# Kernel tuning notes

Measured on AMD Instinct MI355X. Metric: run time of the kernel, lower is better.

The kernel has to match this reference:

```python
import jax, jax.numpy as jnp
import numpy as np
from jax import lax

B, C_IN, H, W = 32, 96, 48, 48
D = C_IN          # d_inner = expand(1) * in_features
K, N, DT_RANK = 2, 16, 6   # k_group, d_state, ceil(D/16)


def setup_inputs() -> dict:
    key = jax.random.key(0)
    ks = jax.random.split(key, 10)
    s = 0.02
    return {
        "x": jax.random.normal(ks[0], (B, C_IN, H, W), jnp.float32),
        "in_proj_w": jax.random.normal(ks[1], (D, C_IN)) * s,
        "in_proj_b": jnp.zeros((D,)),
        "skip_w": jax.random.normal(ks[2], (1, 1, 5)) * s,
        "skip_b": jnp.zeros((1,)),
        "conv2d_w": jax.random.normal(ks[3], (D, 1, 3, 3)) * s,
        "conv2d_b": jnp.zeros((D,)),
        "local_w": jax.random.normal(ks[4], (D, 1, 3, 3)) * s,
        "local_b": jnp.zeros((D,)),
        "bn_gamma": jnp.ones((D,)),
        "bn_beta": jnp.zeros((D,)),
        "x_proj_w": jax.random.normal(ks[5], (K, DT_RANK + 2 * N, D)) * s,
        "dt_projs_w": jax.random.normal(ks[6], (K, D, DT_RANK)) * s,
        "dt_projs_b": jax.random.normal(ks[7], (K, D)) * s,
        "A_logs": jnp.tile(jnp.log(jnp.arange(1, N + 1, dtype=jnp.float32))[None], (K * D, 1)),
        "Ds": jnp.ones((K * D,)),
        "norm_gamma": jnp.ones((D,)),
        "norm_beta": jnp.zeros((D,)),
        "out_proj_w": jax.random.normal(ks[8], (C_IN, D)) * s,
        "out_proj_b": jnp.zeros((C_IN,)),
    }


def _dwconv2d(x, w, bias):
    # depthwise 3x3, NCHW
    y = lax.conv_general_dilated(x, w, (1, 1), "SAME", feature_group_count=x.shape[1],
                                 dimension_numbers=("NCHW", "OIHW", "NCHW"))
    return y + bias[None, :, None, None]


def _forward(x, in_proj_w, in_proj_b, skip_w, skip_b, conv2d_w, conv2d_b,
             local_w, local_b, bn_gamma, bn_beta, x_proj_w, dt_projs_w,
             dt_projs_b, A_logs, Ds, norm_gamma, norm_beta, out_proj_w, out_proj_b):
    b, c, h, w = x.shape
    L = h * w
    x_in = jnp.transpose(x, (0, 2, 3, 1))                       # [B,H,W,C]
    # skip gate: Conv1d(1,1,k=5) over channel axis of the spatial mean
    zm = jnp.mean(x_in, axis=(1, 2))[:, None, :]                # [B,1,C]
    z = lax.conv_general_dilated(zm, skip_w, (1,), "SAME",
                                 dimension_numbers=("NCH", "OIH", "NCH")) + skip_b[None, :, None]
    z = z[:, None]                                              # [B,1,1,C]
    x_feat = jnp.transpose(x_in @ in_proj_w.T + in_proj_b, (0, 3, 1, 2))  # [B,D,H,W]
    x_conv = jax.nn.silu(_dwconv2d(x_feat, conv2d_w, conv2d_b))
    # ---- dynamic center-similarity ordering (computed under no_grad) ----
    xc = lax.stop_gradient(x_conv)
    xf = xc.reshape(b, D, L)
    xn = xf / jnp.maximum(jnp.linalg.norm(xf, axis=1, keepdims=True), 1e-12)
    cf = xc[:, :, h // 2, w // 2]                               # [B,D]
    cn = cf / jnp.maximum(jnp.linalg.norm(cf, axis=1, keepdims=True), 1e-12)
    sim = jnp.einsum("bdl,bd->bl", xn, cn)
    sort_idx = jnp.argsort(-sim, axis=1)                        # descending similarity
    inv_idx = jnp.argsort(sort_idx, axis=1)
    # ---- DynamicCenterScan: sorted sequence and its reverse (k_group=2) ----
    xseq = jnp.take_along_axis(x_conv.reshape(b, D, L), sort_idx[:, None, :], axis=2)
    xs = jnp.stack([xseq, jnp.flip(xseq, -1)], axis=1)          # [B,K,D,L]
    # ---- SS2D selective-scan core ----
    x_dbl = jnp.einsum("bkdl,kcd->bkcl", xs, x_proj_w)
    dts, Bs, Cs = jnp.split(x_dbl, [DT_RANK, DT_RANK + N], axis=2)
    dts = jnp.einsum("bkrl,kdr->bkdl", dts, dt_projs_w)
    dts = jax.nn.softplus(dts + dt_projs_b[None, :, :, None])   # [B,K,D,L]
    A = -jnp.exp(A_logs.reshape(K, D, N))                       # [K,D,N]

    def step(hst, t):
        dt_l, B_l, C_l, x_l = t                                 # [B,K,D],[B,K,N],[B,K,N],[B,K,D]
        dA = jnp.exp(dt_l[..., None] * A)                       # [B,K,D,N]
        hst = dA * hst + (dt_l * x_l)[..., None] * B_l[:, :, None, :]
        y = jnp.einsum("bkdn,bkn->bkd", hst, C_l)
        return hst, y

    tmove = lambda a: jnp.moveaxis(a, -1, 0)
    h0 = jnp.zeros((b, K, D, N), x.dtype)
    _, ys_t = lax.scan(step, h0, (tmove(dts), tmove(Bs), tmove(Cs), tmove(xs)))
    ys = jnp.moveaxis(ys_t, 0, -1) + Ds.reshape(K, D)[None, :, :, None] * xs  # [B,K,D,L]
    # ---- DynamicCenterMerge: un-flip, sum directions, inverse permutation ----
    y = ys[:, 0] + jnp.flip(ys[:, 1], -1)
    y = jnp.take_along_axis(y, inv_idx[:, None, :], axis=2).reshape(b, D, h, w)
    # out_norm: LayerNorm over channels
    yl = jnp.transpose(y, (0, 2, 3, 1))
    mu = jnp.mean(yl, -1, keepdims=True)
    var = jnp.var(yl, -1, keepdims=True)
    yl = (yl - mu) / jnp.sqrt(var + 1e-5) * norm_gamma + norm_beta
    out_mamba = jnp.transpose(yl, (0, 3, 1, 2))
    # local path: depthwise conv + BatchNorm (batch stats, train mode) + SiLU
    lc = _dwconv2d(x_conv, local_w, local_b)
    bm = jnp.mean(lc, (0, 2, 3))
    bv = jnp.var(lc, (0, 2, 3))
    lc = (lc - bm[None, :, None, None]) * (bn_gamma / jnp.sqrt(bv + 1e-5))[None, :, None, None] + bn_beta[None, :, None, None]
    lc = jax.nn.silu(lc)
    out = out_mamba + lc
    # softmax over dim=1 of z (singleton) == all-ones gate; kept for faithfulness
    out = jnp.transpose(out, (0, 2, 3, 1)) * jax.nn.softmax(z, axis=1)
    out = out @ out_proj_w.T + out_proj_b
    return jnp.transpose(out, (0, 3, 1, 2))


def reference(x, in_proj_w, in_proj_b, skip_w, skip_b, conv2d_w, conv2d_b,
              local_w, local_b, bn_gamma, bn_beta, x_proj_w, dt_projs_w,
              dt_projs_b, A_logs, Ds, norm_gamma, norm_beta, out_proj_w, out_proj_b):
    return _forward(x, in_proj_w, in_proj_b, skip_w, skip_b, conv2d_w, conv2d_b,
                    local_w, local_b, bn_gamma, bn_beta, x_proj_w, dt_projs_w,
                    dt_projs_b, A_logs, Ds, norm_gamma, norm_beta, out_proj_w, out_proj_b)
```

## Files before the change

kernel.cpp:

```cpp
#include <hip/hip_runtime.h>
#include <hip/hip_bf16.h>


typedef __hip_bfloat16 bf16;
typedef float v2f __attribute__((ext_vector_type(2)));
typedef float v4f __attribute__((ext_vector_type(4)));
#define SH2(V, a, b) __builtin_shufflevector(V, V, a, b)

__device__ __forceinline__ float b2f(bf16 v) { return __bfloat162float(v); }
__device__ __forceinline__ float ldu(const void* p, int i, bool f32) {
  if (f32) return ((const float*)p)[i];
  return b2f(((const bf16*)p)[i]);
}
__device__ __forceinline__ float rcp_f(float x) { return __builtin_amdgcn_rcpf(x); }

#define LL 2304
#define NSEG 72

#define W_INT  0
#define B_IN   9216
#define W_C2D  9312
#define B_C2D  10176
#define W_LOC  10272
#define B_LOC  11136
#define BN_G   11232
#define BN_B   11328
#define W_XPT  11424
#define W_DT   19104
#define B_DT   20256
#define A2OF   20448
#define DSOF   23520
#define LN_G   23712
#define LN_B   23808
#define W_OUTT 23904
#define B_OUT  33120
#define WBUF_N 33280ul

#define O_WBUF  0ul
#define O_XFEAT 33280ul
#define O_XCONV 7111168ul
#define O_SIM   14189056ul
#define O_SIDX  14262784ul
#define O_XST   14336512ul
#define O_XSTD  21414400ul
#define O_RBUF  28492288ul
#define O_BC    29671936ul
#define O_DSUM  34390528ul
#define O_YMLM  34832896ul
#define O_STATS 41910784ul
#define O_AFLG  41910976ul
#define O_SCSH  41911040ul
#define O_FLAG  41911232ul
#define O_END   41911296ul

__global__ void k_detect(const void* x, float* flag) {
  int i = threadIdx.x;
  bool bad = false;
  const bf16* xb = (const bf16*)x;
#pragma unroll
  for (int r = 0; r < 4; ++r) {
    float v = b2f(xb[r * 64 + i]);
    if (!(fabsf(v) <= 1e4f)) bad = true;
  }
  bool any = __any(bad);
  if (i == 0) flag[0] = any ? 1.f : 0.f;
}

__global__ void k_prep(const void* ipw, const void* ipb, const void* c2w, const void* c2b,
                       const void* lw, const void* lb, const void* bng, const void* bnb,
                       const void* xpw, const void* dtw, const void* dtb, const void* alog,
                       const void* dss, const void* ng, const void* nb, const void* opw,
                       const void* opb, float* wb, const float* flag, float* aflag) {
  bool f = flag[0] > 0.5f;
  int i = blockIdx.x * 256 + threadIdx.x;
  if (i < 9216) {
    int r = i / 96, c = i % 96;
    wb[W_INT + c * 96 + r] = ldu(ipw, i, f);
    wb[W_OUTT + c * 96 + r] = ldu(opw, i, f);
  }
  if (i < 96) {
    wb[B_IN + i] = ldu(ipb, i, f); wb[B_C2D + i] = ldu(c2b, i, f); wb[B_LOC + i] = ldu(lb, i, f);
    wb[BN_G + i] = ldu(bng, i, f); wb[BN_B + i] = ldu(bnb, i, f); wb[LN_G + i] = ldu(ng, i, f);
    wb[LN_B + i] = ldu(nb, i, f); wb[B_OUT + i] = ldu(opb, i, f);
  }
  if (i < 864) { wb[W_C2D + i] = ldu(c2w, i, f); wb[W_LOC + i] = ldu(lw, i, f); }
  if (i < 7296) {
    int k = i / 3648, c = (i / 96) % 38, d = i % 96;
    wb[W_XPT + d * 80 + k * 38 + c] = ldu(xpw, i, f);
  }
  if (i < 1152) wb[W_DT + i] = ldu(dtw, i, f);
  if (i < 192) { wb[B_DT + i] = ldu(dtb, i, f); wb[DSOF + i] = ldu(dss, i, f); }
  if (i < 3072) {
    float av = expf(ldu(alog, i, f));
    wb[A2OF + i] = -av * 1.4426950408889634f;
    int n = i % 16;
    if (fabsf(av - (float)(n + 1)) > 1e-3f * (n + 1)) atomicAdd(aflag, 1.f);
  }
}

__global__ __launch_bounds__(128, 4)
void k_inproj(const void* __restrict__ x, const float* __restrict__ wb,
              float* __restrict__ xfeat, const float* __restrict__ flag) {
  int b = blockIdx.x / 72;
  int rest = blockIdx.x % 72;
  int q = rest / 18;
  int l = (rest % 18) * 128 + threadIdx.x;
  float acc[24];
#pragma unroll
  for (int j = 0; j < 24; ++j) acc[j] = wb[B_IN + q * 24 + j];
  bool f = flag[0] > 0.5f;
  if (f) {
    const float* xf = (const float*)x;
#pragma unroll 2
    for (int c = 0; c < 96; ++c) {
      float xc = xf[(b * 96 + c) * LL + l];
      const float* wr = wb + W_INT + c * 96 + q * 24;
#pragma unroll
      for (int j = 0; j < 24; ++j) acc[j] += xc * wr[j];
    }
  } else {
    const bf16* xb = (const bf16*)x;
#pragma unroll 2
    for (int c = 0; c < 96; ++c) {
      float xc = b2f(xb[(b * 96 + c) * LL + l]);
      const float* wr = wb + W_INT + c * 96 + q * 24;
#pragma unroll
      for (int j = 0; j < 24; ++j) acc[j] += xc * wr[j];
    }
  }
#pragma unroll
  for (int j = 0; j < 24; ++j) xfeat[(b * 96 + q * 24 + j) * LL + l] = acc[j];
}

__global__ __launch_bounds__(256, 8)
void k_conv_silu(const float* __restrict__ xfeat, const float* __restrict__ wb,
                 float* __restrict__ xconv) {
  int t = blockIdx.x * 256 + threadIdx.x;
  int l = t % LL; int d = (t / LL) % 96; int b = t / (LL * 96);
  int h = l / 48, w = l % 48;
  const float* wr = wb + W_C2D + d * 9;
  const float* src = xfeat + (b * 96 + d) * LL;
  float acc = wb[B_C2D + d];
#pragma unroll
  for (int ki = 0; ki < 3; ++ki) {
    int hh = h + ki - 1; if (hh < 0 || hh >= 48) continue;
#pragma unroll
    for (int kj = 0; kj < 3; ++kj) {
      int ww = w + kj - 1; if (ww < 0 || ww >= 48) continue;
      acc += src[hh * 48 + ww] * wr[ki * 3 + kj];
    }
  }
  xconv[t] = acc / (1.f + expf(-acc));
}

__global__ __launch_bounds__(256, 8)
void k_sim(const float* __restrict__ xconv, float* __restrict__ sim) {
  int b = blockIdx.x / 9;
  int l = (blockIdx.x % 9) * 256 + threadIdx.x;
  const float* base = xconv + (size_t)b * 96 * LL;
  float dot = 0, nrm = 0, cn = 0;
  for (int d = 0; d < 96; ++d) {
    float v = base[d * LL + l];
    float c = base[d * LL + 1176];
    dot += v * c; nrm += v * v; cn += c * c;
  }
  float den = fmaxf(sqrtf(nrm), 1e-12f) * fmaxf(sqrtf(cn), 1e-12f);
  sim[b * LL + l] = dot / den;
}

__global__ __launch_bounds__(256, 8)
void k_rank(const float* __restrict__ sim, int* __restrict__ sidx) {
  __shared__ unsigned su[LL];
  int b = blockIdx.x / 36;
  int part = blockIdx.x % 36;
  const float* sp = sim + b * LL;
  for (int i = threadIdx.x; i < LL; i += 256) {
    unsigned u = __float_as_uint(sp[i]);
    u = (u >> 31) ? ~u : (u | 0x80000000u);
    su[i] = u;
  }
  __syncthreads();
  int lq = threadIdx.x >> 2;
  int ch = threadIdx.x & 3;
  int l = part * 64 + lq;
  unsigned ui = su[l];
  int rank = 0;
  const uint4* s4 = (const uint4*)su;
#pragma unroll 4
  for (int it = 0; it < 144; ++it) {
    int m = 4 * it + ch;
    uint4 U = s4[m];
    int j = 4 * m;
    rank += (int)(U.x > ui) + (int)((U.x == ui) & (j + 0 < l));
    rank += (int)(U.y > ui) + (int)((U.y == ui) & (j + 1 < l));
    rank += (int)(U.z > ui) + (int)((U.z == ui) & (j + 2 < l));
    rank += (int)(U.w > ui) + (int)((U.w == ui) & (j + 3 < l));
  }
  rank += __shfl_xor(rank, 1);
  rank += __shfl_xor(rank, 2);
  if (ch == 0) sidx[b * LL + rank] = l;
}

__global__ __launch_bounds__(256, 4)
void k_gather2(const float* __restrict__ xconv, const int* __restrict__ sidx,
               float* __restrict__ xstd, float* __restrict__ xst) {
  __shared__ float tile[64 * 97];
  __shared__ int sp[64];
  int b = blockIdx.x / 36;
  int l0 = (blockIdx.x % 36) * 64;
  if (threadIdx.x < 64) sp[threadIdx.x] = sidx[b * LL + l0 + threadIdx.x];
  __syncthreads();
  const float* base = xconv + (size_t)b * 96 * LL;
#pragma unroll
  for (int it = 0; it < 24; ++it) {
    int idx = it * 256 + threadIdx.x;
    int d = idx / 64, j = idx % 64;
    tile[j * 97 + d] = base[d * LL + sp[j]];
  }
  __syncthreads();
#pragma unroll
  for (int it = 0; it < 24; ++it) {
    int idx = it * 256 + threadIdx.x;
    int r = idx / 96, c = idx % 96;
    xst[((size_t)b * LL + l0 + r) * 96 + c] = tile[r * 97 + c];
  }
#pragma unroll
  for (int it = 0; it < 24; ++it) {
    int idx = it * 256 + threadIdx.x;
    int d = idx / 64, j = idx % 64;
    xstd[((size_t)b * 96 + d) * LL + l0 + j] = tile[j * 97 + d];
  }
}

__global__ __launch_bounds__(256, 4)
void k_tr_ld(const float* __restrict__ in, float* __restrict__ out) {
  __shared__ float tile[64 * 97];
  int b = blockIdx.x / 36;
  int l0 = (blockIdx.x % 36) * 64;
#pragma unroll
  for (int it = 0; it < 24; ++it) {
    int idx = it * 256 + threadIdx.x;
    int r = idx / 96, c = idx % 96;
    tile[r * 97 + c] = in[((size_t)b * LL + l0 + r) * 96 + c];
  }
  __syncthreads();
#pragma unroll
  for (int it = 0; it < 24; ++it) {
    int idx = it * 256 + threadIdx.x;
    int d = idx / 64, j = idx % 64;
    out[((size_t)b * 96 + d) * LL + l0 + j] = tile[j * 97 + d];
  }
}

__global__ __launch_bounds__(128, 4)
void k_xdbl(const float* __restrict__ xstd, const float* __restrict__ wb,
            float* __restrict__ rbuf, float* __restrict__ bc) {
  int kq = blockIdx.x / 576;
  int r = blockIdx.x % 576;
  int b = r / 18;
  int l = (r % 18) * 128 + threadIdx.x;
  float acc[38];
#pragma unroll
  for (int j = 0; j < 38; ++j) acc[j] = 0.f;
#pragma unroll 2
  for (int c = 0; c < 96; ++c) {
    float xc = xstd[((size_t)b * 96 + c) * LL + l];
    const float* wr = wb + W_XPT + c * 80 + kq * 38;
#pragma unroll
    for (int j = 0; j < 38; ++j) acc[j] += xc * wr[j];
  }
  int lout = kq ? (LL - 1 - l) : l;
  float4* r4 = (float4*)(rbuf + ((size_t)(b * 2 + kq) * LL + lout) * 8);
  r4[0] = make_float4(acc[0], acc[1], acc[2], acc[3]);
  r4[1] = make_float4(acc[4], acc[5], 0.f, 0.f);
  float4* b4 = (float4*)(bc + ((size_t)(b * 2 + kq) * LL + lout) * 32);
#pragma unroll
  for (int i = 0; i < 8; ++i)
    b4[i] = make_float4(acc[6 + 4 * i], acc[7 + 4 * i], acc[8 + 4 * i], acc[9 + 4 * i]);
}

__global__ __launch_bounds__(192, 3)
void k_scan1(const float* __restrict__ rbuf, const float* __restrict__ bc,
             const float* __restrict__ xst, const float* __restrict__ wb,
             float* __restrict__ dsum, float* __restrict__ hend,
             const float* __restrict__ aflag) {
  __shared__ float sbc[2][512];
  __shared__ float srr[2][256];
  int sub = threadIdx.x / 96;
  int tid = threadIdx.x - sub * 96;
  int unit = blockIdx.x * 2 + sub;
  int s = unit % 72; int k = (unit / 72) % 2; int b = unit / 144;
  int lbase = (b * 2 + k) * LL + s * 32;
  long long lk0 = k ? (LL - 1 - s * 32) : (s * 32);
  long long stp = k ? -96 : 96;
  const float* xp = xst + (size_t)b * LL * 96 + lk0 * 96 + tid;
  float xv[32];
#pragma unroll
  for (int t = 0; t < 32; ++t) xv[t] = xp[t * stp];
  {
    const float4* bsrc = (const float4*)(bc + (size_t)lbase * 32);
    float4* bdst = (float4*)sbc[sub];
    for (int i = tid; i < 128; i += 96) {
      int l = i >> 2, c = i & 3;
      bdst[i] = bsrc[l * 8 + c];
    }
    const float4* rsrc = (const float4*)(rbuf + (size_t)lbase * 8);
    float4* rdst = (float4*)srr[sub];
    if (tid < 64) rdst[tid] = rsrc[tid];
  }
  __syncthreads();
  int d = tid;
  float wd[6];
#pragma unroll
  for (int j = 0; j < 6; ++j) wd[j] = wb[W_DT + (k * 96 + d) * 6 + j];
  float bd = wb[B_DT + k * 96 + d];
  float ds = 0.f;
  v2f h2[8];
#pragma unroll
  for (int j = 0; j < 8; ++j) h2[j] = (v2f){0.f, 0.f};
  bool fast = (aflag[0] == 0.f);
  if (fast) {
    const v4f* bq4 = (const v4f*)sbc[sub];
    const v4f* rq4 = (const v4f*)srr[sub];
#pragma unroll
    for (int t = 0; t < 32; ++t) {
      v4f r0 = rq4[t * 2], r1 = rq4[t * 2 + 1];
      float a = bd + r0.x * wd[0] + r0.y * wd[1] + r0.z * wd[2]
                   + r0.w * wd[3] + r1.x * wd[4] + r1.y * wd[5];
      float ea = __expf(a);
      float p1 = rcp_f(1.f + ea);
      float dtv = (a > 20.f) ? a : -0.69314718055994531f * __log2f(p1);
      ds += dtv;
      float dtx = dtv * xv[t];
      v2f dt2 = {dtx, dtx};
      float p2s = p1 * p1;
      v2f P1 = {p1, p2s};
      v2f P2 = P1 * (v2f){p2s, p2s};
      float p4s = P2.y;
      v2f P3 = P1 * (v2f){p4s, p4s};
      v2f P4 = P2 * (v2f){p4s, p4s};
      float p8s = P4.y;
      v2f P5 = P1 * (v2f){p8s, p8s};
      v2f P6 = P2 * (v2f){p8s, p8s};
      v2f P7 = P3 * (v2f){p8s, p8s};
      v2f P8 = P4 * (v2f){p8s, p8s};
      v4f B0 = bq4[t * 4 + 0], B1 = bq4[t * 4 + 1];
      v4f B2 = bq4[t * 4 + 2], B3 = bq4[t * 4 + 3];
      h2[0] = P1 * h2[0] + dt2 * SH2(B0, 0, 1);
      h2[1] = P2 * h2[1] + dt2 * SH2(B0, 2, 3);
      h2[2] = P3 * h2[2] + dt2 * SH2(B1, 0, 1);
      h2[3] = P4 * h2[3] + dt2 * SH2(B1, 2, 3);
      h2[4] = P5 * h2[4] + dt2 * SH2(B2, 0, 1);
      h2[5] = P6 * h2[5] + dt2 * SH2(B2, 2, 3);
      h2[6] = P7 * h2[6] + dt2 * SH2(B3, 0, 1);
      h2[7] = P8 * h2[7] + dt2 * SH2(B3, 2, 3);
    }
  } else {
    float a2[16], hh[16];
#pragma unroll
    for (int n = 0; n < 16; ++n) { a2[n] = wb[A2OF + (k * 96 + d) * 16 + n]; hh[n] = 0.f; }
#pragma unroll 4
    for (int t = 0; t < 32; ++t) {
      const float* rr = &srr[sub][t * 8];
      float a = bd + rr[0] * wd[0] + rr[1] * wd[1] + rr[2] * wd[2]
                   + rr[3] * wd[3] + rr[4] * wd[4] + rr[5] * wd[5];
      float dtv = (a > 20.f) ? a : log1pf(expf(a));
      ds += dtv;
      float dtx = dtv * xv[t];
      const float* bcl = &sbc[sub][t * 16];
#pragma unroll
      for (int n = 0; n < 16; ++n) hh[n] = exp2f(dtv * a2[n]) * hh[n] + dtx * bcl[n];
    }
#pragma unroll
    for (int j = 0; j < 8; ++j) h2[j] = (v2f){hh[2 * j], hh[2 * j + 1]};
  }
  dsum[((b * 2 + k) * 96 + d) * NSEG + s] = ds;
  float4* ho = (float4*)(hend + (((size_t)(b * 2 + k) * NSEG + s) * 96 + d) * 16);
  ho[0] = make_float4(h2[0].x, h2[0].y, h2[1].x, h2[1].y);
  ho[1] = make_float4(h2[2].x, h2[2].y, h2[3].x, h2[3].y);
  ho[2] = make_float4(h2[4].x, h2[4].y, h2[5].x, h2[5].y);
  ho[3] = make_float4(h2[6].x, h2[6].y, h2[7].x, h2[7].y);
}

__global__ __launch_bounds__(256, 4)
void k_scan2(const float* __restrict__ dsum, const float* __restrict__ hend,
             const float* __restrict__ wb, float* __restrict__ hstart) {
  int t = blockIdx.x * 256 + threadIdx.x;
  int n = t % 16; int d = (t / 16) % 96; int k = (t / 1536) % 2; int b = t / 3072;
  float a2 = wb[A2OF + (k * 96 + d) * 16 + n];
  float h = 0.f;
  int rowd = ((b * 2 + k) * 96 + d) * NSEG;
#pragma unroll 8
  for (int s = 0; s < NSEG; ++s) {
    size_t idx = (((size_t)(b * 2 + k) * NSEG + s) * 96 + d) * 16 + n;
    hstart[idx] = h;
    h = exp2f(a2 * dsum[rowd + s]) * h + hend[idx];
  }
}

__global__ __launch_bounds__(192, 3)
void k_scan3ln(const float* __restrict__ rbuf, const float* __restrict__ bc,
               const float* __restrict__ xst, const float* __restrict__ wb,
               const float* __restrict__ hstart, const int* __restrict__ sidx,
               float* __restrict__ ymlm, const float* __restrict__ aflag) {
  __shared__ float yA[32 * 97];
  __shared__ float yB[32 * 97];
  __shared__ float sbc[2][1024];
  __shared__ float srr[2][256];
  __shared__ float smu[32], srs[32];
  int b = blockIdx.x / NSEG;
  int u = blockIdx.x % NSEG;
  int t = threadIdx.x;
  int sub = t / 96;
  int d = t - sub * 96;
  int k = sub;
  int seg = sub ? (NSEG - 1 - u) : u;
  int lbase = (b * 2 + k) * LL + seg * 32;
  long long lk0 = k ? (LL - 1 - seg * 32) : (seg * 32);
  long long stp = k ? -96 : 96;
  const float* xp = xst + (size_t)b * LL * 96 + lk0 * 96 + d;
  float xv[32];
#pragma unroll
  for (int i = 0; i < 32; ++i) xv[i] = xp[i * stp];
  {
    const float4* bsrc = (const float4*)(bc + (size_t)lbase * 32);
    float4* bdst = (float4*)sbc[sub];
    for (int i = d; i < 256; i += 96) bdst[i] = bsrc[i];
    const float4* rsrc = (const float4*)(rbuf + (size_t)lbase * 8);
    float4* rdst = (float4*)srr[sub];
    if (d < 64) rdst[d] = rsrc[d];
  }
  __syncthreads();
  {
    float* yacc = sub ? yB : yA;
    float wd[6];
#pragma unroll
    for (int j = 0; j < 6; ++j) wd[j] = wb[W_DT + (k * 96 + d) * 6 + j];
    float bd = wb[B_DT + k * 96 + d];
    float Dv = wb[DSOF + k * 96 + d];
    const float* hi = hstart + (((size_t)(b * 2 + k) * NSEG + seg) * 96 + d) * 16;
    bool fast = (aflag[0] == 0.f);
    if (fast) {
      const v4f* hi4 = (const v4f*)hi;
      v4f H0 = hi4[0], H1 = hi4[1], H2 = hi4[2], H3 = hi4[3];
      v2f h2[8];
      h2[0] = SH2(H0, 0, 1); h2[1] = SH2(H0, 2, 3);
      h2[2] = SH2(H1, 0, 1); h2[3] = SH2(H1, 2, 3);
      h2[4] = SH2(H2, 0, 1); h2[5] = SH2(H2, 2, 3);
      h2[6] = SH2(H3, 0, 1); h2[7] = SH2(H3, 2, 3);
      const v4f* bq4 = (const v4f*)sbc[sub];
      const v4f* rq4 = (const v4f*)srr[sub];
#pragma unroll
      for (int i = 0; i < 32; ++i) {
        v4f r0 = rq4[i * 2], r1 = rq4[i * 2 + 1];
        float a = bd + r0.x * wd[0] + r0.y * wd[1] + r0.z * wd[2]
                     + r0.w * wd[3] + r1.x * wd[4] + r1.y * wd[5];
        float ea = __expf(a);
        float p1 = rcp_f(1.f + ea);
        float dtv = (a > 20.f) ? a : -0.69314718055994531f * __log2f(p1);
        float dtx = dtv * xv[i];
        v2f dt2 = {dtx, dtx};
        float p2s = p1 * p1;
        v2f P1 = {p1, p2s};
        v2f P2 = P1 * (v2f){p2s, p2s};
        float p4s = P2.y;
        v2f P3 = P1 * (v2f){p4s, p4s};
        v2f P4 = P2 * (v2f){p4s, p4s};
        float p8s = P4.y;
        v2f P5 = P1 * (v2f){p8s, p8s};
        v2f P6 = P2 * (v2f){p8s, p8s};
        v2f P7 = P3 * (v2f){p8s, p8s};
        v2f P8 = P4 * (v2f){p8s, p8s};
        v4f B0 = bq4[i * 8 + 0], B1 = bq4[i * 8 + 1];
        v4f B2 = bq4[i * 8 + 2], B3 = bq4[i * 8 + 3];
        v4f C0 = bq4[i * 8 + 4], C1 = bq4[i * 8 + 5];
        v4f C2 = bq4[i * 8 + 6], C3 = bq4[i * 8 + 7];
        v2f y2;
        h2[0] = P1 * h2[0] + dt2 * SH2(B0, 0, 1); y2  = h2[0] * SH2(C0, 0, 1);
        h2[1] = P2 * h2[1] + dt2 * SH2(B0, 2, 3); y2 += h2[1] * SH2(C0, 2, 3);
        h2[2] = P3 * h2[2] + dt2 * SH2(B1, 0, 1); y2 += h2[2] * SH2(C1, 0, 1);
        h2[3] = P4 * h2[3] + dt2 * SH2(B1, 2, 3); y2 += h2[3] * SH2(C1, 2, 3);
        h2[4] = P5 * h2[4] + dt2 * SH2(B2, 0, 1); y2 += h2[4] * SH2(C2, 0, 1);
        h2[5] = P6 * h2[5] + dt2 * SH2(B2, 2, 3); y2 += h2[5] * SH2(C2, 2, 3);
        h2[6] = P7 * h2[6] + dt2 * SH2(B3, 0, 1); y2 += h2[6] * SH2(C3, 0, 1);
        h2[7] = P8 * h2[7] + dt2 * SH2(B3, 2, 3); y2 += h2[7] * SH2(C3, 2, 3);
        int qloc = k ? (31 - i) : i;
        yacc[qloc * 97 + d] = y2.x + y2.y + Dv * xv[i];
      }
    } else {
      float a2[16], hh[16];
#pragma unroll
      for (int n = 0; n < 16; ++n) { a2[n] = wb[A2OF + (k * 96 + d) * 16 + n]; hh[n] = hi[n]; }
#pragma unroll 4
      for (int i = 0; i < 32; ++i) {
        const float* rr = &srr[sub][i * 8];
        float a = bd + rr[0] * wd[0] + rr[1] * wd[1] + rr[2] * wd[2]
                     + rr[3] * wd[3] + rr[4] * wd[4] + rr[5] * wd[5];
        float dtv = (a > 20.f) ? a : log1pf(expf(a));
        float dtx = dtv * xv[i];
        const float* bcl = &sbc[sub][i * 32];
        float y = 0.f;
#pragma unroll
        for (int n = 0; n < 16; ++n) {
          hh[n] = exp2f(dtv * a2[n]) * hh[n] + dtx * bcl[n];
          y += hh[n] * bcl[16 + n];
        }
        int qloc = k ? (31 - i) : i;
        yacc[qloc * 97 + d] = y + Dv * xv[i];
      }
    }
  }
  __syncthreads();
  {
    float* p1 = &srr[0][0];
    float* p2 = &srr[0][0] + 192;
    int r = t & 31, c0 = (t >> 5) * 16;
    float s = 0, ss = 0;
#pragma unroll
    for (int j = 0; j < 16; ++j) {
      float v = yA[r * 97 + c0 + j] + yB[r * 97 + c0 + j];
      s += v; ss += v * v;
    }
    p1[t] = s; p2[t] = ss;
  }
  __syncthreads();
  if (t < 32) {
    const float* p1 = &srr[0][0];
    const float* p2 = &srr[0][0] + 192;
    float s = 0, ss = 0;
#pragma unroll
    for (int g = 0; g < 6; ++g) { s += p1[g * 32 + t]; ss += p2[g * 32 + t]; }
    float mu = s * (1.f / 96.f);
    float var = ss * (1.f / 96.f) - mu * mu;
    smu[t] = mu;
    srs[t] = rsqrtf(var + 1e-5f);
  }
  __syncthreads();
  {
    int r = t & 31, c0 = (t >> 5) * 16;
    int q = u * 32 + r;
    int p = sidx[b * LL + q];
    float mu = smu[r], rs = srs[r];
    float tmp[16];
#pragma unroll
    for (int j = 0; j < 16; ++j) {
      int dd = c0 + j;
      tmp[j] = (yA[r * 97 + dd] + yB[r * 97 + dd] - mu) * rs * wb[LN_G + dd] + wb[LN_B + dd];
    }
    float4* o4 = (float4*)(ymlm + ((size_t)b * LL + p) * 96 + c0);
    o4[0] = make_float4(tmp[0], tmp[1], tmp[2], tmp[3]);
    o4[1] = make_float4(tmp[4], tmp[5], tmp[6], tmp[7]);
    o4[2] = make_float4(tmp[8], tmp[9], tmp[10], tmp[11]);
    o4[3] = make_float4(tmp[12], tmp[13], tmp[14], tmp[15]);
  }
}

__global__ __launch_bounds__(256, 8)
void k_convlc_bn(const float* __restrict__ xconv, const float* __restrict__ wb,
                 float* __restrict__ lcbuf, float* __restrict__ stats) {
  int bd = blockIdx.x;
  int b = bd / 96, d = bd % 96;
  const float* src = xconv + (size_t)(b * 96 + d) * LL;
  const float* wr = wb + W_LOC + d * 9;
  float bias = wb[B_LOC + d];
  float s1 = 0, s2 = 0;
  for (int l = threadIdx.x; l < LL; l += 256) {
    int h = l / 48, w = l % 48;
    float acc = bias;
#pragma unroll
    for (int ki = 0; ki < 3; ++ki) {
      int hh = h + ki - 1; if (hh < 0 || hh >= 48) continue;
#pragma unroll
      for (int kj = 0; kj < 3; ++kj) {
        int ww = w + kj - 1; if (ww < 0 || ww >= 48) continue;
        acc += src[hh * 48 + ww] * wr[ki * 3 + kj];
      }
    }
    lcbuf[(size_t)(b * 96 + d) * LL + l] = acc;
    s1 += acc; s2 += acc * acc;
  }
  __shared__ float r1[256], r2[256];
  r1[threadIdx.x] = s1; r2[threadIdx.x] = s2; __syncthreads();
  for (int o = 128; o > 0; o >>= 1) {
    if (threadIdx.x < o) { r1[threadIdx.x] += r1[threadIdx.x + o]; r2[threadIdx.x] += r2[threadIdx.x + o]; }
    __syncthreads();
  }
  if (threadIdx.x == 0) { atomicAdd(&stats[d], r1[0]); atomicAdd(&stats[96 + d], r2[0]); }
}

__global__ void k_bnfin(const float* __restrict__ stats, const float* __restrict__ wb,
                        float* __restrict__ scsh) {
  int d = threadIdx.x; if (d >= 96) return;
  float mean = stats[d] * (1.f / 73728.f);
  float var = stats[96 + d] * (1.f / 73728.f) - mean * mean;
  float sc = wb[BN_G + d] * rsqrtf(var + 1e-5f);
  scsh[d] = sc; scsh[96 + d] = wb[BN_B + d] - mean * sc;
}

__global__ __launch_bounds__(128, 4)
void k_final(const float* __restrict__ lcbuf, const float* __restrict__ ymdm,
             const float* __restrict__ wb, const float* __restrict__ scsh,
             void* __restrict__ out, const float* __restrict__ flag) {
  int b = blockIdx.x / 72;
  int rest = blockIdx.x % 72;
  int q = rest / 18;
  int l = (rest % 18) * 128 + threadIdx.x;
  float acc[24];
#pragma unroll
  for (int j = 0; j < 24; ++j) acc[j] = wb[B_OUT + q * 24 + j];
#pragma unroll 2
  for (int d = 0; d < 96; ++d) {
    float lc = lcbuf[((size_t)b * 96 + d) * LL + l] * scsh[d] + scsh[96 + d];
    float vd = lc * rcp_f(1.f + __expf(-lc)) + ymdm[((size_t)b * 96 + d) * LL + l];
    const float* wr = wb + W_OUTT + d * 96 + q * 24;
#pragma unroll
    for (int j = 0; j < 24; ++j) acc[j] += vd * wr[j];
  }
  bool f = flag[0] > 0.5f;
  if (f) {
    float* of = (float*)out;
#pragma unroll
    for (int j = 0; j < 24; ++j) of[(b * 96 + q * 24 + j) * LL + l] = acc[j];
  } else {
    bf16* ob = (bf16*)out;
#pragma unroll
    for (int j = 0; j < 24; ++j) ob[(b * 96 + q * 24 + j) * LL + l] = __float2bfloat16(acc[j]);
  }
}

extern "C" void kernel_launch(void* const* d_in, const int* in_sizes, int n_in,
                              void* d_out, int out_size, void* d_ws, size_t ws_size,
                              hipStream_t stream) {
  if (ws_size < O_END * sizeof(float)) return;
  float* ws = (float*)d_ws;
  float* wb    = ws + O_WBUF;
  float* xfeat = ws + O_XFEAT;
  float* xconv = ws + O_XCONV;
  float* sim   = ws + O_SIM;
  int*   sidx  = (int*)(ws + O_SIDX);
  float* xst   = ws + O_XST;
  float* xstd  = ws + O_XSTD;
  float* rbuf  = ws + O_RBUF;
  float* bc    = ws + O_BC;
  float* dsum  = ws + O_DSUM;
  float* ymlm  = ws + O_YMLM;
  float* stats = ws + O_STATS;
  float* aflag = ws + O_AFLG;
  float* scsh  = ws + O_SCSH;
  float* flag  = ws + O_FLAG;
  float* hend   = xfeat;
  float* hstart = xstd;
  float* ymdm   = xfeat;
  float* lcbuf  = xst;

  hipMemsetAsync(stats, 0, 256 * sizeof(float), stream);
  k_detect<<<1, 64, 0, stream>>>(d_in[0], flag);
  k_prep<<<36, 256, 0, stream>>>(
      d_in[1], d_in[2], d_in[5], d_in[6], d_in[7], d_in[8], d_in[9], d_in[10],
      d_in[11], d_in[12], d_in[13], d_in[14], d_in[15], d_in[16], d_in[17], d_in[18],
      d_in[19], wb, flag, aflag);
  k_inproj<<<2304, 128, 0, stream>>>(d_in[0], wb, xfeat, flag);
  k_conv_silu<<<27648, 256, 0, stream>>>(xfeat, wb, xconv);
  k_sim<<<288, 256, 0, stream>>>(xconv, sim);
  k_rank<<<1152, 256, 0, stream>>>(sim, sidx);
  k_gather2<<<1152, 256, 0, stream>>>(xconv, sidx, xstd, xst);
  k_xdbl<<<1152, 128, 0, stream>>>(xstd, wb, rbuf, bc);
  k_scan1<<<2304, 192, 0, stream>>>(rbuf, bc, xst, wb, dsum, hend, aflag);
  k_scan2<<<384, 256, 0, stream>>>(dsum, hend, wb, hstart);
  k_scan3ln<<<2304, 192, 0, stream>>>(rbuf, bc, xst, wb, hstart, sidx, ymlm, aflag);
  k_tr_ld<<<1152, 256, 0, stream>>>(ymlm, ymdm);
  k_convlc_bn<<<3072, 256, 0, stream>>>(xconv, wb, lcbuf, stats);
  k_bnfin<<<1, 96, 0, stream>>>(stats, wb, scsh);
  k_final<<<2304, 128, 0, stream>>>(lcbuf, ymdm, wb, scsh, d_out, flag);
}
```

Before: 502.4 us.

## Vectorize conv_silu by four, split xdbl outputs across blocks, fold BN finalize into final

The depthwise conv+SiLU kernel now has each thread compute four adjacent outputs and store them as one float4, which cuts launch count and index math. k_xdbl is split into two block halves, one for the first 22 and one for the remaining 16 projection outputs, which doubles parallelism and lowers register pressure at the cost of reading the input twice. The k_bnfin launch is removed and the BN scale and shift are recomputed per channel inside k_final, saving a tiny kernel launch but adding redundant per-thread math.

Result: slower. 515.2 us (+2.5%).

```diff
diff --git a/kernel.cpp b/kernel.cpp
--- a/kernel.cpp
+++ b/kernel.cpp
@@ -136,21 +136,34 @@
 void k_conv_silu(const float* __restrict__ xfeat, const float* __restrict__ wb,
                  float* __restrict__ xconv) {
   int t = blockIdx.x * 256 + threadIdx.x;
-  int l = t % LL; int d = (t / LL) % 96; int b = t / (LL * 96);
-  int h = l / 48, w = l % 48;
+  int lq = t % 576; int d = (t / 576) % 96; int b = t / (576 * 96);
+  int l0 = lq * 4;
+  int h = l0 / 48, w0 = l0 % 48;
   const float* wr = wb + W_C2D + d * 9;
   const float* src = xfeat + (b * 96 + d) * LL;
-  float acc = wb[B_C2D + d];
+  float bias = wb[B_C2D + d];
+  float acc[4] = {bias, bias, bias, bias};
 #pragma unroll
   for (int ki = 0; ki < 3; ++ki) {
     int hh = h + ki - 1; if (hh < 0 || hh >= 48) continue;
+    const float* row = src + hh * 48;
 #pragma unroll
     for (int kj = 0; kj < 3; ++kj) {
-      int ww = w + kj - 1; if (ww < 0 || ww >= 48) continue;
-      acc += src[hh * 48 + ww] * wr[ki * 3 + kj];
-    }
-  }
-  xconv[t] = acc / (1.f + expf(-acc));
+      float wv = wr[ki * 3 + kj];
+#pragma unroll
+      for (int u = 0; u < 4; ++u) {
+        int ww = w0 + u + kj - 1;
+        if (ww < 0 || ww >= 48) continue;
+        acc[u] += row[ww] * wv;
+      }
+    }
+  }
+  float4 o;
+  o.x = acc[0] / (1.f + expf(-acc[0]));
+  o.y = acc[1] / (1.f + expf(-acc[1]));
+  o.z = acc[2] / (1.f + expf(-acc[2]));
+  o.w = acc[3] / (1.f + expf(-acc[3]));
+  *(float4*)(xconv + (size_t)(b * 96 + d) * LL + l0) = o;
 }
 
 __global__ __launch_bounds__(256, 8)
@@ -255,28 +268,47 @@
 __global__ __launch_bounds__(128, 4)
 void k_xdbl(const float* __restrict__ xstd, const float* __restrict__ wb,
             float* __restrict__ rbuf, float* __restrict__ bc) {
-  int kq = blockIdx.x / 576;
-  int r = blockIdx.x % 576;
+  int half = blockIdx.x / 1152;
+  int r2 = blockIdx.x % 1152;
+  int kq = r2 / 576;
+  int r = r2 % 576;
   int b = r / 18;
   int l = (r % 18) * 128 + threadIdx.x;
-  float acc[38];
-#pragma unroll
-  for (int j = 0; j < 38; ++j) acc[j] = 0.f;
+  int lout = kq ? (LL - 1 - l) : l;
+  if (half == 0) {
+    float acc[22];
+#pragma unroll
+    for (int j = 0; j < 22; ++j) acc[j] = 0.f;
 #pragma unroll 2
-  for (int c = 0; c < 96; ++c) {
-    float xc = xstd[((size_t)b * 96 + c) * LL + l];
-    const float* wr = wb + W_XPT + c * 80 + kq * 38;
-#pragma unroll
-    for (int j = 0; j < 38; ++j) acc[j] += xc * wr[j];
-  }
-  int lout = kq ? (LL - 1 - l) : l;
-  float4* r4 = (float4*)(rbuf + ((size_t)(b * 2 + kq) * LL + lout) * 8);
-  r4[0] = make_float4(acc[0], acc[1], acc[2], acc[3]);
-  r4[1] = make_float4(acc[4], acc[5], 0.f, 0.f);
-  float4* b4 = (float4*)(bc + ((size_t)(b * 2 + kq) * LL + lout) * 32);
-#pragma unroll
-  for (int i = 0; i < 8; ++i)
-    b4[i] = make_float4(acc[6 + 4 * i], acc[7 + 4 * i], acc[8 + 4 * i], acc[9 + 4 * i]);
+    for (int c = 0; c < 96; ++c) {
+      float xc = xstd[((size_t)b * 96 + c) * LL + l];
+      const float* wr = wb + W_XPT + c * 80 + kq * 38;
+#pragma unroll
+      for (int j = 0; j < 22; ++j) acc[j] += xc * wr[j];
+    }
+    float4* r4 = (float4*)(rbuf + ((size_t)(b * 2 + kq) * LL + lout) * 8);
+    r4[0] = make_float4(acc[0], acc[1], acc[2], acc[3]);
+    r4[1] = make_float4(acc[4], acc[5], 0.f, 0.f);
+    float4* b4 = (float4*)(bc + ((size_t)(b * 2 + kq) * LL + lout) * 32);
+#pragma unroll
+    for (int i = 0; i < 4; ++i)
+      b4[i] = make_float4(acc[6 + 4 * i], acc[7 + 4 * i], acc[8 + 4 * i], acc[9 + 4 * i]);
+  } else {
+    float acc[16];
+#pragma unroll
+    for (int j = 0; j < 16; ++j) acc[j] = 0.f;
+#pragma unroll 2
+    for (int c = 0; c < 96; ++c) {
+      float xc = xstd[((size_t)b * 96 + c) * LL + l];
+      const float* wr = wb + W_XPT + c * 80 + kq * 38 + 22;
+#pragma unroll
+      for (int j = 0; j < 16; ++j) acc[j] += xc * wr[j];
+    }
+    float4* b4 = (float4*)(bc + ((size_t)(b * 2 + kq) * LL + lout) * 32);
+#pragma unroll
+    for (int i = 0; i < 4; ++i)
+      b4[4 + i] = make_float4(acc[4 * i], acc[4 * i + 1], acc[4 * i + 2], acc[4 * i + 3]);
+  }
 }
 
 __global__ __launch_bounds__(192, 3)
@@ -588,18 +620,9 @@
   if (threadIdx.x == 0) { atomicAdd(&stats[d], r1[0]); atomicAdd(&stats[96 + d], r2[0]); }
 }
 
-__global__ void k_bnfin(const float* __restrict__ stats, const float* __restrict__ wb,
-                        float* __restrict__ scsh) {
-  int d = threadIdx.x; if (d >= 96) return;
-  float mean = stats[d] * (1.f / 73728.f);
-  float var = stats[96 + d] * (1.f / 73728.f) - mean * mean;
-  float sc = wb[BN_G + d] * rsqrtf(var + 1e-5f);
-  scsh[d] = sc; scsh[96 + d] = wb[BN_B + d] - mean * sc;
-}
-
 __global__ __launch_bounds__(128, 4)
 void k_final(const float* __restrict__ lcbuf, const float* __restrict__ ymdm,
-             const float* __restrict__ wb, const float* __restrict__ scsh,
+             const float* __restrict__ wb, const float* __restrict__ stats,
              void* __restrict__ out, const float* __restrict__ flag) {
   int b = blockIdx.x / 72;
   int rest = blockIdx.x % 72;
@@ -610,7 +633,11 @@
   for (int j = 0; j < 24; ++j) acc[j] = wb[B_OUT + q * 24 + j];
 #pragma unroll 2
   for (int d = 0; d < 96; ++d) {
-    float lc = lcbuf[((size_t)b * 96 + d) * LL + l] * scsh[d] + scsh[96 + d];
+    float mean = stats[d] * (1.f / 73728.f);
+    float var = stats[96 + d] * (1.f / 73728.f) - mean * mean;
+    float sc = wb[BN_G + d] * rsqrtf(var + 1e-5f);
+    float sh = wb[BN_B + d] - mean * sc;
+    float lc = lcbuf[((size_t)b * 96 + d) * LL + l] * sc + sh;
     float vd = lc * rcp_f(1.f + __expf(-lc)) + ymdm[((size_t)b * 96 + d) * LL + l];
     const float* wr = wb + W_OUTT + d * 96 + q * 24;
 #pragma unroll
@@ -646,7 +673,6 @@
   float* ymlm  = ws + O_YMLM;
   float* stats = ws + O_STATS;
   float* aflag = ws + O_AFLG;
-  float* scsh  = ws + O_SCSH;
   float* flag  = ws + O_FLAG;
   float* hend   = xfeat;
   float* hstart = xstd;
@@ -660,16 +686,15 @@
       d_in[11], d_in[12], d_in[13], d_in[14], d_in[15], d_in[16], d_in[17], d_in[18],
       d_in[19], wb, flag, aflag);
   k_inproj<<<2304, 128, 0, stream>>>(d_in[0], wb, xfeat, flag);
-  k_conv_silu<<<27648, 256, 0, stream>>>(xfeat, wb, xconv);
+  k_conv_silu<<<6912, 256, 0, stream>>>(xfeat, wb, xconv);
   k_sim<<<288, 256, 0, stream>>>(xconv, sim);
   k_rank<<<1152, 256, 0, stream>>>(sim, sidx);
   k_gather2<<<1152, 256, 0, stream>>>(xconv, sidx, xstd, xst);
-  k_xdbl<<<1152, 128, 0, stream>>>(xstd, wb, rbuf, bc);
+  k_xdbl<<<2304, 128, 0, stream>>>(xstd, wb, rbuf, bc);
   k_scan1<<<2304, 192, 0, stream>>>(rbuf, bc, xst, wb, dsum, hend, aflag);
   k_scan2<<<384, 256, 0, stream>>>(dsum, hend, wb, hstart);
   k_scan3ln<<<2304, 192, 0, stream>>>(rbuf, bc, xst, wb, hstart, sidx, ymlm, aflag);
   k_tr_ld<<<1152, 256, 0, stream>>>(ymlm, ymdm);
   k_convlc_bn<<<3072, 256, 0, stream>>>(xconv, wb, lcbuf, stats);
-  k_bnfin<<<1, 96, 0, stream>>>(stats, wb, scsh);
-  k_final<<<2304, 128, 0, stream>>>(lcbuf, ymdm, wb, scsh, d_out, flag);
-}
+  k_final<<<2304, 128, 0, stream>>>(lcbuf, ymdm, wb, stats, d_out, flag);
+}
```
